# Performance work log

Measured on AMD Instinct MI355X. Metric: run time of the kernel, lower is better.

Reference implementation:

```python
import jax, jax.numpy as jnp
import numpy as np

B, N, FIN, FOUT = 16, 128, 128, 256   # batch, atoms(=max_atom), in_features, out_features
EOUT, BIN, BOUT, CI, L1 = 64, 14, 64, 64, 256


def _rnn_dir(x, wih, whh, bih, bhh):
    # x: [B, T, I]; torch nn.RNN step: h = tanh(x @ Wih^T + bih + h @ Whh^T + bhh)
    h0 = jnp.zeros((x.shape[0], whh.shape[0]), x.dtype)
    def step(h, xt):
        h = jnp.tanh(xt @ wih.T + bih + h @ whh.T + bhh)
        return h, h
    _, ys = jax.lax.scan(step, h0, jnp.swapaxes(x, 0, 1))
    return jnp.swapaxes(ys, 0, 1)  # [B, T, H]


def _bi_rnn(x, wih_f, whh_f, bih_f, bhh_f, wih_b, whh_b, bih_b, bhh_b):
    fwd = _rnn_dir(x, wih_f, whh_f, bih_f, bhh_f)
    bwd = _rnn_dir(x[:, ::-1, :], wih_b, whh_b, bih_b, bhh_b)[:, ::-1, :]
    return jnp.concatenate([fwd, bwd], axis=-1)  # [B, T, 2H]


def setup_inputs() -> dict:
    key = jax.random.key(0)
    ks = jax.random.split(key, 24)
    g = lambda i, shape, s=0.05: (jax.random.normal(ks[i], shape, jnp.float32) * s)
    return {
        "x": g(0, (B, N, FIN), 1.0),
        "adj": jax.random.randint(ks[1], (B, N, N), 0, 2).astype(jnp.int32),
        "w_edge": g(2, (B, N, N, BIN), 1.0),
        "W": g(3, (FIN, FOUT)),
        "a": g(4, (2 * FOUT, EOUT)),
        "wfc_w": g(5, (BIN, BOUT)), "wfc_b": g(6, (BOUT,)),
        "fc_w": g(7, (EOUT + BOUT, 1)), "fc_b": g(8, (1,)),
        "fcc_w": g(9, (FOUT, 1)), "fcc_b": g(10, (1,)),
        "wih_f": g(11, (CI, N)), "whh_f": g(12, (CI, CI)), "bih_f": g(13, (CI,)), "bhh_f": g(14, (CI,)),
        "wih_b": g(15, (CI, N)), "whh_b": g(16, (CI, CI)), "bih_b": g(17, (CI,)), "bhh_b": g(18, (CI,)),
        "fco_w": g(19, (2 * CI + FOUT, L1)), "fco_b": g(20, (L1,)),
    }


def reference(x, adj, w_edge, W, a, wfc_w, wfc_b, fc_w, fc_b, fcc_w, fcc_b,
              wih_f, whh_f, bih_f, bhh_f, wih_b, whh_b, bih_b, bhh_b, fco_w, fco_b):
    h = x @ W  # [B, N, FOUT]
    # faithful reproduction of the repeat/cat(dim=1)/view trick
    t1 = jnp.tile(h, (1, 1, N)).reshape(B, N * N, FOUT)  # row i*N+j = h_i
    t2 = jnp.tile(h, (1, N, 1))                          # row i*N+j = h_j
    atom_trans = jnp.concatenate([t1, t2], axis=1).reshape(B, N, N, 2 * FOUT)
    e = atom_trans @ a                                   # [B, N, N, EOUT]
    wproj = w_edge @ wfc_w + wfc_b                       # [B, N, N, BOUT]
    e = jax.nn.leaky_relu(jnp.concatenate([e, wproj], axis=3))
    e = (e @ fc_w + fc_b)[..., 0]                        # [B, N, N]
    att = jax.nn.softmax(jnp.where(adj > 0, e, jnp.float32(-9e15)), axis=2)
    # dropout is identity in eval mode
    at_in = att[..., None] * h[:, :, None, :]            # [B, N, N, FOUT], h_i broadcast over j
    hn = jax.nn.leaky_relu((at_in @ fcc_w + fcc_b)[..., 0])  # [B, N, N]
    hn = jax.nn.leaky_relu(_bi_rnn(hn, wih_f, whh_f, bih_f, bhh_f, wih_b, whh_b, bih_b, bhh_b))
    h1 = jnp.einsum('bij,bjf->bif', att, h)              # [B, N, FOUT]
    out = jnp.concatenate([hn, h1], axis=2) @ fco_w + fco_b  # [B, N, L1]
    return jax.nn.elu(out)
```

## Files before the change

### kernel.cpp

```cpp
#include <hip/hip_runtime.h>
#include <hip/hip_bf16.h>

#define DEV static __device__ __forceinline__

constexpr int B=16, N=128, FIN=128, FOUT=256, EOUT=64, BINW=14, BOUT=64, CI=64, L1=256;

constexpr int O_H   = 0;
constexpr int O_P   = O_H  + B*N*FOUT;
constexpr int O_Q   = O_P  + B*N*EOUT;
constexpr int O_S   = O_Q  + B*N*EOUT;
constexpr int O_SU  = O_S  + B*N;
constexpr int O_SV  = O_SU + B*N;
constexpr int O_ATT = O_SV + B*N;
constexpr int O_ZF  = O_ATT+ B*N*N;
constexpr int O_ZB  = O_ZF + B*N*CI;
constexpr int O_RF  = O_ZB + B*N*CI;
constexpr int O_RB  = O_RF + B*N*CI;

DEV float bf16_to_f32(unsigned short u){
  unsigned int x = ((unsigned int)u) << 16; float f;
  __builtin_memcpy(&f, &x, 4); return f;
}
DEV void bf2x(unsigned int u, float& lo, float& hi){
  unsigned int a = u << 16, b = u & 0xFFFF0000u;
  __builtin_memcpy(&lo, &a, 4); __builtin_memcpy(&hi, &b, 4);
}
DEV float lrelu(float x){ return x > 0.f ? x : 0.01f * x; }
DEV float bcastf(float v, int lane){
  return __builtin_bit_cast(float, __builtin_amdgcn_readlane(__builtin_bit_cast(int, v), lane));
}
DEV float ldf(const void* p, int i, int m){
  return m ? bf16_to_f32(((const unsigned short*)p)[i]) : ((const float*)p)[i];
}
DEV int blk_mode(const void* x, int nt, int tid){
  const unsigned short* u = (const unsigned short*)x;
  int e = (u[tid & 255] >> 7) & 0xFF;
  int cnt = __syncthreads_count(e >= 100 && e <= 140);
  return cnt * 4 >= nt * 3;
}

__global__ __launch_bounds__(256) void k_h_pq(const void* __restrict__ xr,
                                              const void* __restrict__ Wp,
                                              const void* __restrict__ Ap,
                                              const void* __restrict__ fccwp,
                                              float* __restrict__ ws){
  int blk = blockIdx.x, tid = threadIdx.x;
  int b = blk >> 4, i0 = (blk & 15) * 8;
  __shared__ __align__(16) float xl[8*FIN];
  __shared__ __align__(16) float hrow[8*FOUT];
  __shared__ float red[32];
  int mode = blk_mode(xr, 256, tid);
  if (mode){
    const unsigned short* xu = (const unsigned short*)xr + (size_t)(b*N + i0)*FIN;
    for (int t = tid; t < 8*FIN/8; t += 256){
      uint4 u4 = ((const uint4*)xu)[t];
      float* o = &xl[t*8];
      bf2x(u4.x,o[0],o[1]); bf2x(u4.y,o[2],o[3]); bf2x(u4.z,o[4],o[5]); bf2x(u4.w,o[6],o[7]);
    }
  } else {
    const float* xf = (const float*)xr + (size_t)(b*N + i0)*FIN;
    for (int t4 = tid; t4 < 8*FIN/4; t4 += 256)
      *(float4*)&xl[t4*4] = ((const float4*)xf)[t4];
  }
  __syncthreads();
  int f = tid;
  float acc[8] = {0,0,0,0,0,0,0,0};
  if (mode){
    const unsigned short* Wu = (const unsigned short*)Wp;
    for (int c = 0; c < FIN; c += 4){
      float w0 = bf16_to_f32(Wu[(c+0)*FOUT + f]);
      float w1 = bf16_to_f32(Wu[(c+1)*FOUT + f]);
      float w2 = bf16_to_f32(Wu[(c+2)*FOUT + f]);
      float w3 = bf16_to_f32(Wu[(c+3)*FOUT + f]);
      #pragma unroll
      for (int r = 0; r < 8; ++r){
        float4 x4 = *(const float4*)&xl[r*FIN + c];
        acc[r] += x4.x*w0 + x4.y*w1 + x4.z*w2 + x4.w*w3;
      }
    }
  } else {
    const float* Wf = (const float*)Wp;
    for (int c = 0; c < FIN; c += 4){
      float w0 = Wf[(c+0)*FOUT + f];
      float w1 = Wf[(c+1)*FOUT + f];
      float w2 = Wf[(c+2)*FOUT + f];
      float w3 = Wf[(c+3)*FOUT + f];
      #pragma unroll
      for (int r = 0; r < 8; ++r){
        float4 x4 = *(const float4*)&xl[r*FIN + c];
        acc[r] += x4.x*w0 + x4.y*w1 + x4.z*w2 + x4.w*w3;
      }
    }
  }
  float fw = ldf(fccwp, f, mode);
  #pragma unroll
  for (int r = 0; r < 8; ++r){
    ws[O_H + (b*N + i0 + r)*FOUT + f] = acc[r];
    hrow[r*FOUT + f] = acc[r];
  }
  #pragma unroll
  for (int r = 0; r < 8; ++r){
    float v = acc[r] * fw;
    for (int off = 32; off; off >>= 1) v += __shfl_down(v, off);
    if ((tid & 63) == 0) red[(tid >> 6)*8 + r] = v;
  }
  __syncthreads();
  if (tid < 8){
    float s = red[tid] + red[8+tid] + red[16+tid] + red[24+tid];
    ws[O_S + b*N + i0 + tid] = s;
  }
  {
    int o = tid & 63, which = (tid >> 6) & 1, hh = tid >> 7;
    float a4[4] = {0.f,0.f,0.f,0.f};
    if (mode){
      const unsigned short* Au = (const unsigned short*)Ap;
      for (int c = 0; c < FOUT; c += 4){
        float w0 = bf16_to_f32(Au[(which*FOUT + c+0)*EOUT + o]);
        float w1 = bf16_to_f32(Au[(which*FOUT + c+1)*EOUT + o]);
        float w2 = bf16_to_f32(Au[(which*FOUT + c+2)*EOUT + o]);
        float w3 = bf16_to_f32(Au[(which*FOUT + c+3)*EOUT + o]);
        #pragma unroll
        for (int r = 0; r < 4; ++r){
          float4 h4 = *(const float4*)&hrow[(hh*4+r)*FOUT + c];
          a4[r] += h4.x*w0 + h4.y*w1 + h4.z*w2 + h4.w*w3;
        }
      }
    } else {
      const float* Af = (const float*)Ap;
      for (int c = 0; c < FOUT; c += 4){
        float w0 = Af[(which*FOUT + c+0)*EOUT + o];
        float w1 = Af[(which*FOUT + c+1)*EOUT + o];
        float w2 = Af[(which*FOUT + c+2)*EOUT + o];
        float w3 = Af[(which*FOUT + c+3)*EOUT + o];
        #pragma unroll
        for (int r = 0; r < 4; ++r){
          float4 h4 = *(const float4*)&hrow[(hh*4+r)*FOUT + c];
          a4[r] += h4.x*w0 + h4.y*w1 + h4.z*w2 + h4.w*w3;
        }
      }
    }
    int ob = which ? O_Q : O_P;
    #pragma unroll
    for (int r = 0; r < 4; ++r)
      ws[ob + (b*N + i0 + hh*4 + r)*EOUT + o] = a4[r];
  }
}

__global__ __launch_bounds__(64) void k_susv(const void* __restrict__ xr,
                                             const void* __restrict__ fcwp,
                                             float* __restrict__ ws){
  int blk = blockIdx.x; int b = blk >> 7, r = blk & 127; int o = threadIdx.x;
  int mode = blk_mode(xr, 64, o);
  float fw = ldf(fcwp, o, mode);
  const float* R = ws;
  float u = R[O_P + (b*N + r)*EOUT + o] + R[O_Q + (b*N + r)*EOUT + o];
  float t1 = lrelu(u) * fw;
  int j2 = (2*r) & 127;
  float v = R[O_P + (b*N + j2)*EOUT + o] + R[O_Q + (b*N + j2 + 1)*EOUT + o];
  float t2 = lrelu(v) * fw;
  for (int off = 32; off; off >>= 1){ t1 += __shfl_down(t1, off); t2 += __shfl_down(t2, off); }
  if (o == 0){ ws[O_SU + b*N + r] = t1; ws[O_SV + b*N + r] = t2; }
}

struct AttArgs { const void *we,*x,*wfcw,*wfcb,*fcw,*fcb,*fccb,*wihf,*bihf,*bhhf,*wihb,*bihb,*bhhb; };

__global__ __launch_bounds__(128) void k_att(AttArgs A, const int* __restrict__ adj,
                                             float* __restrict__ ws){
  int blk = blockIdx.x; int b = blk >> 7, i = blk & 127; int tid = threadIdx.x;
  __shared__ __align__(16) float wel[N*BINW];
  __shared__ __align__(16) float hnp[N];
  __shared__ __align__(16) float wfcwl[BINW*BOUT];
  __shared__ __align__(16) float wfcbl[BOUT];
  __shared__ __align__(16) float fcw2l[BOUT];
  __shared__ float red2[2];
  int mode = blk_mode(A.x, 128, tid);
  for (int t = tid; t < BINW*BOUT; t += 128) wfcwl[t] = ldf(A.wfcw, t, mode);
  if (tid < BOUT){ wfcbl[tid] = ldf(A.wfcb, tid, mode); fcw2l[tid] = ldf(A.fcw, EOUT + tid, mode); }
  if (mode){
    const unsigned short* weu = (const unsigned short*)A.we + (size_t)(b*N + i)*N*BINW;
    for (int t = tid; t < N*BINW/8; t += 128){
      uint4 q = ((const uint4*)weu)[t];
      float* o = &wel[t*8];
      bf2x(q.x,o[0],o[1]); bf2x(q.y,o[2],o[3]); bf2x(q.z,o[4],o[5]); bf2x(q.w,o[6],o[7]);
    }
  } else {
    const float* wef = (const float*)A.we + (size_t)(b*N + i)*N*BINW;
    for (int t4 = tid; t4 < N*BINW/4; t4 += 128)
      *(float4*)&wel[t4*4] = ((const float4*)wef)[t4];
  }
  __syncthreads();
  int j = tid;
  float wr[BINW];
  #pragma unroll
  for (int t = 0; t < BINW; ++t) wr[t] = wel[j*BINW + t];
  float wcon = 0.f;
  for (int o = 0; o < BOUT; o += 4){
    float4 bb = *(const float4*)&wfcbl[o];
    float w0 = bb.x, w1 = bb.y, w2 = bb.z, w3 = bb.w;
    #pragma unroll
    for (int t = 0; t < BINW; ++t){
      float4 w4 = *(const float4*)&wfcwl[t*BOUT + o];
      w0 = fmaf(wr[t], w4.x, w0); w1 = fmaf(wr[t], w4.y, w1);
      w2 = fmaf(wr[t], w4.z, w2); w3 = fmaf(wr[t], w4.w, w3);
    }
    float4 f4 = *(const float4*)&fcw2l[o];
    wcon += lrelu(w0)*f4.x + lrelu(w1)*f4.y + lrelu(w2)*f4.z + lrelu(w3)*f4.w;
  }
  const float* R = ws;
  float econ = (i < 64) ? R[O_SU + b*N + 2*i + (j >= 64 ? 1 : 0)]
                        : R[O_SV + b*N + j];
  float etot = econ + wcon + ldf(A.fcb, 0, mode);
  float m = (adj[(b*N + i)*N + j] > 0) ? etot : -9e15f;
  float mx = m;
  for (int off = 32; off; off >>= 1) mx = fmaxf(mx, __shfl_xor(mx, off));
  if ((tid & 63) == 0) red2[tid >> 6] = mx;
  __syncthreads();
  mx = fmaxf(red2[0], red2[1]);
  float ev = expf(m - mx);
  float sum = ev;
  for (int off = 32; off; off >>= 1) sum += __shfl_xor(sum, off);
  __syncthreads();
  if ((tid & 63) == 0) red2[tid >> 6] = sum;
  __syncthreads();
  sum = red2[0] + red2[1];
  float att = ev / sum;
  ws[O_ATT + (b*N + i)*N + j] = att;
  float sbi = R[O_S + b*N + i];
  hnp[j] = lrelu(att * sbi + ldf(A.fccb, 0, mode));
  __syncthreads();
  {
    int d = tid >> 6, c = tid & 63;
    float acc = ldf(d ? A.bihb : A.bihf, c, mode) + ldf(d ? A.bhhb : A.bhhf, c, mode);
    const void* wihp = d ? A.wihb : A.wihf;
    if (mode){
      const uint4* wq = (const uint4*)((const unsigned short*)wihp + c*N);
      #pragma unroll 4
      for (int k = 0; k < N; k += 8){
        uint4 q = wq[k >> 3];
        float w0,w1,w2,w3,w4,w5,w6,w7;
        bf2x(q.x,w0,w1); bf2x(q.y,w2,w3); bf2x(q.z,w4,w5); bf2x(q.w,w6,w7);
        float4 h0 = *(const float4*)&hnp[k];
        float4 h1 = *(const float4*)&hnp[k+4];
        acc += h0.x*w0 + h0.y*w1 + h0.z*w2 + h0.w*w3
             + h1.x*w4 + h1.y*w5 + h1.z*w6 + h1.w*w7;
      }
    } else {
      const float* wf = (const float*)wihp + c*N;
      #pragma unroll 8
      for (int k = 0; k < N; k += 4){
        float4 h4 = *(const float4*)&hnp[k];
        float4 w4 = *(const float4*)&wf[k];
        acc += h4.x*w4.x + h4.y*w4.y + h4.z*w4.z + h4.w*w4.w;
      }
    }
    ws[(d ? O_ZB : O_ZF) + (b*N + i)*CI + c] = acc;
  }
}

__global__ __launch_bounds__(64, 1) void k_rnn(const void* __restrict__ xr,
                                               const void* __restrict__ whhf,
                                               const void* __restrict__ whhb,
                                               float* __restrict__ ws){
  int blk = blockIdx.x; int d = blk >> 4, b = blk & 15; int c = threadIdx.x;
  int mode = blk_mode(xr, 64, c);
  const void* whhp = d ? whhb : whhf;
  const int zb = (d ? O_ZB : O_ZF) + b*N*CI;
  const int ob = (d ? O_RB : O_RF) + b*N*CI;
  __shared__ __align__(16) float zo[N*CI];
  float wreg[CI];
  if (mode){
    const uint4* wq = (const uint4*)((const unsigned short*)whhp + c*CI);
    #pragma unroll
    for (int k = 0; k < CI; k += 8){
      uint4 q = wq[k >> 3];
      bf2x(q.x,wreg[k+0],wreg[k+1]); bf2x(q.y,wreg[k+2],wreg[k+3]);
      bf2x(q.z,wreg[k+4],wreg[k+5]); bf2x(q.w,wreg[k+6],wreg[k+7]);
    }
  } else {
    const float* wf = (const float*)whhp + c*CI;
    #pragma unroll
    for (int k = 0; k < CI; k += 4){
      float4 w4 = *(const float4*)&wf[k];
      wreg[k]=w4.x; wreg[k+1]=w4.y; wreg[k+2]=w4.z; wreg[k+3]=w4.w;
    }
  }
  for (int it = 0; it < N*CI/4; it += 64)
    *(float4*)&zo[(it + c)*4] = *(const float4*)&ws[zb + (it + c)*4];
  const int step = d ? -1 : 1;
  int tt = d ? (N-1) : 0;
  float hv = 0.f;
  float z = zo[tt*CI + c];
  for (int t = 0; t < N; ++t){
    int ti = tt + step; ti = ti < 0 ? 0 : (ti > N-1 ? N-1 : ti);
    float znext = zo[ti*CI + c];
    float s[CI];
    #pragma unroll
    for (int k = 0; k < CI; ++k) s[k] = bcastf(hv, k);
#if __has_builtin(__builtin_amdgcn_sched_barrier)
    __builtin_amdgcn_sched_barrier(0);
#endif
    float a0 = z, a1 = 0.f, a2 = 0.f, a3 = 0.f;
    #pragma unroll
    for (int k = 0; k < CI; k += 4){
      a0 = fmaf(s[k+0], wreg[k+0], a0);
      a1 = fmaf(s[k+1], wreg[k+1], a1);
      a2 = fmaf(s[k+2], wreg[k+2], a2);
      a3 = fmaf(s[k+3], wreg[k+3], a3);
    }
    float x = (a0+a1)+(a2+a3);
    x = fminf(15.f, fmaxf(-15.f, x));
    float p = __expf(2.f * x);
    hv = (p - 1.f) * __builtin_amdgcn_rcpf(p + 1.f);
    zo[tt*CI + c] = hv;
    z = znext;
    tt += step;
  }
  for (int it = 0; it < N*CI/4; it += 64)
    *(float4*)&ws[ob + (it + c)*4] = *(const float4*)&zo[(it + c)*4];
}

__global__ __launch_bounds__(256) void k_out(const void* __restrict__ xr,
                                             const void* __restrict__ fcowp,
                                             const void* __restrict__ fcobp,
                                             const float* __restrict__ R, void* dout){
  int blk = blockIdx.x, tid = threadIdx.x;
  int b = blk >> 4, i0 = (blk & 15) * 8;
  constexpr int KW = 2*CI + FOUT;
  __shared__ __align__(16) float attT[N*8];
  __shared__ __align__(16) float inl[8*KW];
  int mode = blk_mode(xr, 256, tid);
  for (int t = tid; t < 8*N; t += 256){
    int r = t >> 7, k = t & 127;
    attT[k*8 + r] = R[O_ATT + (b*N + i0 + r)*N + k];
  }
  for (int t = tid; t < 8*2*CI; t += 256){
    int r = t >> 7, k = t & 127;
    int row = b*N + i0 + r;
    inl[r*KW + k] = (k < CI) ? lrelu(R[O_RF + row*CI + k])
                             : lrelu(R[O_RB + row*CI + (k - CI)]);
  }
  __syncthreads();
  int f = tid;
  {
    float acc[8] = {0,0,0,0,0,0,0,0};
    for (int k = 0; k < N; ++k){
      float hv = R[O_H + (b*N + k)*FOUT + f];
      float4 a0 = *(const float4*)&attT[k*8];
      float4 a1 = *(const float4*)&attT[k*8 + 4];
      acc[0] += a0.x*hv; acc[1] += a0.y*hv; acc[2] += a0.z*hv; acc[3] += a0.w*hv;
      acc[4] += a1.x*hv; acc[5] += a1.y*hv; acc[6] += a1.z*hv; acc[7] += a1.w*hv;
    }
    #pragma unroll
    for (int r = 0; r < 8; ++r) inl[r*KW + 2*CI + f] = acc[r];
  }
  __syncthreads();
  int l = tid;
  float bias = ldf(fcobp, l, mode);
  float acc[8];
  #pragma unroll
  for (int r = 0; r < 8; ++r) acc[r] = bias;
  if (mode){
    const unsigned short* fu = (const unsigned short*)fcowp;
    for (int k = 0; k < KW; k += 4){
      float w0 = bf16_to_f32(fu[(k+0)*L1 + l]);
      float w1 = bf16_to_f32(fu[(k+1)*L1 + l]);
      float w2 = bf16_to_f32(fu[(k+2)*L1 + l]);
      float w3 = bf16_to_f32(fu[(k+3)*L1 + l]);
      #pragma unroll
      for (int r = 0; r < 8; ++r){
        float4 v = *(const float4*)&inl[r*KW + k];
        acc[r] += v.x*w0 + v.y*w1 + v.z*w2 + v.w*w3;
      }
    }
  } else {
    const float* ff = (const float*)fcowp;
    for (int k = 0; k < KW; k += 4){
      float w0 = ff[(k+0)*L1 + l];
      float w1 = ff[(k+1)*L1 + l];
      float w2 = ff[(k+2)*L1 + l];
      float w3 = ff[(k+3)*L1 + l];
      #pragma unroll
      for (int r = 0; r < 8; ++r){
        float4 v = *(const float4*)&inl[r*KW + k];
        acc[r] += v.x*w0 + v.y*w1 + v.z*w2 + v.w*w3;
      }
    }
  }
  #pragma unroll
  for (int r = 0; r < 8; ++r){
    float o = acc[r] > 0.f ? acc[r] : expm1f(acc[r]);
    int idx = (b*N + i0 + r)*L1 + l;
    if (mode) ((__hip_bfloat16*)dout)[idx] = __float2bfloat16(o);
    else      ((float*)dout)[idx] = o;
  }
}

extern "C" void kernel_launch(void* const* d_in, const int* in_sizes, int n_in,
                              void* d_out, int out_size, void* d_ws, size_t ws_size,
                              hipStream_t stream){
  (void)in_sizes; (void)n_in; (void)out_size; (void)ws_size;
  float* ws = (float*)d_ws;
  AttArgs A;
  A.we = d_in[2]; A.x = d_in[0]; A.wfcw = d_in[5]; A.wfcb = d_in[6];
  A.fcw = d_in[7]; A.fcb = d_in[8]; A.fccb = d_in[10];
  A.wihf = d_in[11]; A.bihf = d_in[13]; A.bhhf = d_in[14];
  A.wihb = d_in[15]; A.bihb = d_in[17]; A.bhhb = d_in[18];
  hipLaunchKernelGGL(k_h_pq, dim3(256),  dim3(256), 0, stream,
                     d_in[0], d_in[3], d_in[4], d_in[9], ws);
  hipLaunchKernelGGL(k_susv, dim3(B*N),  dim3(64),  0, stream, d_in[0], d_in[7], ws);
  hipLaunchKernelGGL(k_att,  dim3(B*N),  dim3(128), 0, stream, A, (const int*)d_in[1], ws);
  hipLaunchKernelGGL(k_rnn,  dim3(32),   dim3(64),  0, stream,
                     d_in[0], d_in[12], d_in[16], ws);
  hipLaunchKernelGGL(k_out,  dim3(256),  dim3(256), 0, stream,
                     d_in[0], d_in[19], d_in[20], ws, d_out);
}
```

Measured before the change: 212.9 us.

## Fuse susv into h_pq, pack two attention rows per block, overlap h1 with RNN

The separate k_susv kernel is folded into k_h_pq, so P/Q projections stay in shared memory and the su/sv scores come from a block-local reduction instead of a global round trip. k_att now processes two attention rows per 256-thread block. The att@h matmul (h1) moves out of k_out into a combined kernel in which 32 blocks run the serial RNN while the other 224 blocks compute h1 in parallel, hiding it behind the RNN latency. This removes one launch and some global traffic, but the fused su/sv indexing is subtle and adds an extra h1 workspace buffer.

Measured after the change: 205.4 us (median of 2 runs). -3.5%, faster.

```diff
diff --git a/kernel.cpp b/kernel.cpp
--- a/kernel.cpp
+++ b/kernel.cpp
@@ -6,9 +6,7 @@
 constexpr int B=16, N=128, FIN=128, FOUT=256, EOUT=64, BINW=14, BOUT=64, CI=64, L1=256;
 
 constexpr int O_H   = 0;
-constexpr int O_P   = O_H  + B*N*FOUT;
-constexpr int O_Q   = O_P  + B*N*EOUT;
-constexpr int O_S   = O_Q  + B*N*EOUT;
+constexpr int O_S   = O_H  + B*N*FOUT;
 constexpr int O_SU  = O_S  + B*N;
 constexpr int O_SV  = O_SU + B*N;
 constexpr int O_ATT = O_SV + B*N;
@@ -16,6 +14,7 @@
 constexpr int O_ZB  = O_ZF + B*N*CI;
 constexpr int O_RF  = O_ZB + B*N*CI;
 constexpr int O_RB  = O_RF + B*N*CI;
+constexpr int O_H1  = O_RB + B*N*CI;
 
 DEV float bf16_to_f32(unsigned short u){
   unsigned int x = ((unsigned int)u) << 16; float f;
@@ -43,11 +42,14 @@
                                               const void* __restrict__ Wp,
                                               const void* __restrict__ Ap,
                                               const void* __restrict__ fccwp,
+                                              const void* __restrict__ fcwp,
                                               float* __restrict__ ws){
   int blk = blockIdx.x, tid = threadIdx.x;
   int b = blk >> 4, i0 = (blk & 15) * 8;
   __shared__ __align__(16) float xl[8*FIN];
   __shared__ __align__(16) float hrow[8*FOUT];
+  __shared__ __align__(16) float pl[8*EOUT];
+  __shared__ __align__(16) float ql[8*EOUT];
   __shared__ float red[32];
   int mode = blk_mode(xr, 256, tid);
   if (mode){
@@ -139,60 +141,63 @@
         }
       }
     }
-    int ob = which ? O_Q : O_P;
+    float* dst = which ? ql : pl;
     #pragma unroll
-    for (int r = 0; r < 4; ++r)
-      ws[ob + (b*N + i0 + hh*4 + r)*EOUT + o] = a4[r];
-  }
-}
-
-__global__ __launch_bounds__(64) void k_susv(const void* __restrict__ xr,
-                                             const void* __restrict__ fcwp,
+    for (int r = 0; r < 4; ++r) dst[(hh*4+r)*EOUT + o] = a4[r];
+  }
+  __syncthreads();
+  {
+    int o = tid & 63, w = tid >> 6;
+    float fw2 = ldf(fcwp, o, mode);
+    float s1 = lrelu(pl[w*EOUT + o]     + ql[w*EOUT + o])     * fw2;
+    float s2 = lrelu(pl[(w+4)*EOUT + o] + ql[(w+4)*EOUT + o]) * fw2;
+    float s3 = lrelu(pl[(2*w)*EOUT + o] + ql[(2*w+1)*EOUT + o]) * fw2;
+    for (int off = 32; off; off >>= 1){
+      s1 += __shfl_down(s1, off); s2 += __shfl_down(s2, off); s3 += __shfl_down(s3, off);
+    }
+    if (o == 0){
+      ws[O_SU + b*N + i0 + w]     = s1;
+      ws[O_SU + b*N + i0 + w + 4] = s2;
+      int r1 = (i0 + 2*w) >> 1;
+      ws[O_SV + b*N + r1]      = s3;
+      ws[O_SV + b*N + r1 + 64] = s3;
+    }
+  }
+}
+
+struct AttArgs { const void *we,*x,*wfcw,*wfcb,*fcw,*fcb,*fccb,*wihf,*bihf,*bhhf,*wihb,*bihb,*bhhb; };
+
+__global__ __launch_bounds__(256) void k_att(AttArgs A, const int* __restrict__ adj,
                                              float* __restrict__ ws){
-  int blk = blockIdx.x; int b = blk >> 7, r = blk & 127; int o = threadIdx.x;
-  int mode = blk_mode(xr, 64, o);
-  float fw = ldf(fcwp, o, mode);
-  const float* R = ws;
-  float u = R[O_P + (b*N + r)*EOUT + o] + R[O_Q + (b*N + r)*EOUT + o];
-  float t1 = lrelu(u) * fw;
-  int j2 = (2*r) & 127;
-  float v = R[O_P + (b*N + j2)*EOUT + o] + R[O_Q + (b*N + j2 + 1)*EOUT + o];
-  float t2 = lrelu(v) * fw;
-  for (int off = 32; off; off >>= 1){ t1 += __shfl_down(t1, off); t2 += __shfl_down(t2, off); }
-  if (o == 0){ ws[O_SU + b*N + r] = t1; ws[O_SV + b*N + r] = t2; }
-}
-
-struct AttArgs { const void *we,*x,*wfcw,*wfcb,*fcw,*fcb,*fccb,*wihf,*bihf,*bhhf,*wihb,*bihb,*bhhb; };
-
-__global__ __launch_bounds__(128) void k_att(AttArgs A, const int* __restrict__ adj,
-                                             float* __restrict__ ws){
-  int blk = blockIdx.x; int b = blk >> 7, i = blk & 127; int tid = threadIdx.x;
-  __shared__ __align__(16) float wel[N*BINW];
-  __shared__ __align__(16) float hnp[N];
+  int blk = blockIdx.x, tid = threadIdx.x;
+  int half = tid >> 7, j = tid & 127, wv = (tid >> 6) & 1;
+  int tau = blk*2 + half;
+  int b = tau >> 7, i = tau & 127;
+  __shared__ __align__(16) float wel[2][N*BINW];
+  __shared__ __align__(16) float hnp[2][N];
   __shared__ __align__(16) float wfcwl[BINW*BOUT];
   __shared__ __align__(16) float wfcbl[BOUT];
   __shared__ __align__(16) float fcw2l[BOUT];
-  __shared__ float red2[2];
-  int mode = blk_mode(A.x, 128, tid);
-  for (int t = tid; t < BINW*BOUT; t += 128) wfcwl[t] = ldf(A.wfcw, t, mode);
+  __shared__ float red2[2][2];
+  int mode = blk_mode(A.x, 256, tid);
+  for (int t = tid; t < BINW*BOUT; t += 256) wfcwl[t] = ldf(A.wfcw, t, mode);
   if (tid < BOUT){ wfcbl[tid] = ldf(A.wfcb, tid, mode); fcw2l[tid] = ldf(A.fcw, EOUT + tid, mode); }
   if (mode){
     const unsigned short* weu = (const unsigned short*)A.we + (size_t)(b*N + i)*N*BINW;
-    for (int t = tid; t < N*BINW/8; t += 128){
+    for (int t = j; t < N*BINW/8; t += 128){
       uint4 q = ((const uint4*)weu)[t];
-      float* o = &wel[t*8];
+      float* o = &wel[half][t*8];
       bf2x(q.x,o[0],o[1]); bf2x(q.y,o[2],o[3]); bf2x(q.z,o[4],o[5]); bf2x(q.w,o[6],o[7]);
     }
   } else {
     const float* wef = (const float*)A.we + (size_t)(b*N + i)*N*BINW;
-    for (int t4 = tid; t4 < N*BINW/4; t4 += 128)
-      *(float4*)&wel[t4*4] = ((const float4*)wef)[t4];
-  }
-  __syncthreads();
-  int j = tid;
+    for (int t4 = j; t4 < N*BINW/4; t4 += 128)
+      *(float4*)&wel[half][t4*4] = ((const float4*)wef)[t4];
+  }
+  __syncthreads();
   float wr[BINW];
   #pragma unroll
-  for (int t = 0; t < BINW; ++t) wr[t] = wel[j*BINW + t];
+  for (int t = 0; t < BINW; ++t) wr[t] = wel[half][j*BINW + t];
   float wcon = 0.f;
   for (int o = 0; o < BOUT; o += 4){
     float4 bb = *(const float4*)&wfcbl[o];
@@ -213,23 +218,23 @@
   float m = (adj[(b*N + i)*N + j] > 0) ? etot : -9e15f;
   float mx = m;
   for (int off = 32; off; off >>= 1) mx = fmaxf(mx, __shfl_xor(mx, off));
-  if ((tid & 63) == 0) red2[tid >> 6] = mx;
-  __syncthreads();
-  mx = fmaxf(red2[0], red2[1]);
+  if ((tid & 63) == 0) red2[half][wv] = mx;
+  __syncthreads();
+  mx = fmaxf(red2[half][0], red2[half][1]);
   float ev = expf(m - mx);
   float sum = ev;
   for (int off = 32; off; off >>= 1) sum += __shfl_xor(sum, off);
   __syncthreads();
-  if ((tid & 63) == 0) red2[tid >> 6] = sum;
-  __syncthreads();
-  sum = red2[0] + red2[1];
+  if ((tid & 63) == 0) red2[half][wv] = sum;
+  __syncthreads();
+  sum = red2[half][0] + red2[half][1];
   float att = ev / sum;
   ws[O_ATT + (b*N + i)*N + j] = att;
   float sbi = R[O_S + b*N + i];
-  hnp[j] = lrelu(att * sbi + ldf(A.fccb, 0, mode));
+  hnp[half][j] = lrelu(att * sbi + ldf(A.fccb, 0, mode));
   __syncthreads();
   {
-    int d = tid >> 6, c = tid & 63;
+    int d = wv, c = tid & 63;
     float acc = ldf(d ? A.bihb : A.bihf, c, mode) + ldf(d ? A.bhhb : A.bhhf, c, mode);
     const void* wihp = d ? A.wihb : A.wihf;
     if (mode){
@@ -239,8 +244,8 @@
         uint4 q = wq[k >> 3];
         float w0,w1,w2,w3,w4,w5,w6,w7;
         bf2x(q.x,w0,w1); bf2x(q.y,w2,w3); bf2x(q.z,w4,w5); bf2x(q.w,w6,w7);
-        float4 h0 = *(const float4*)&hnp[k];
-        float4 h1 = *(const float4*)&hnp[k+4];
+        float4 h0 = *(const float4*)&hnp[half][k];
+        float4 h1 = *(const float4*)&hnp[half][k+4];
         acc += h0.x*w0 + h0.y*w1 + h0.z*w2 + h0.w*w3
              + h1.x*w4 + h1.y*w5 + h1.z*w6 + h1.w*w7;
       }
@@ -248,7 +253,7 @@
       const float* wf = (const float*)wihp + c*N;
       #pragma unroll 8
       for (int k = 0; k < N; k += 4){
-        float4 h4 = *(const float4*)&hnp[k];
+        float4 h4 = *(const float4*)&hnp[half][k];
         float4 w4 = *(const float4*)&wf[k];
         acc += h4.x*w4.x + h4.y*w4.y + h4.z*w4.z + h4.w*w4.w;
       }
@@ -257,66 +262,97 @@
   }
 }
 
-__global__ __launch_bounds__(64, 1) void k_rnn(const void* __restrict__ xr,
-                                               const void* __restrict__ whhf,
-                                               const void* __restrict__ whhb,
-                                               float* __restrict__ ws){
-  int blk = blockIdx.x; int d = blk >> 4, b = blk & 15; int c = threadIdx.x;
-  int mode = blk_mode(xr, 64, c);
-  const void* whhp = d ? whhb : whhf;
-  const int zb = (d ? O_ZB : O_ZF) + b*N*CI;
-  const int ob = (d ? O_RB : O_RF) + b*N*CI;
-  __shared__ __align__(16) float zo[N*CI];
-  float wreg[CI];
-  if (mode){
-    const uint4* wq = (const uint4*)((const unsigned short*)whhp + c*CI);
-    #pragma unroll
-    for (int k = 0; k < CI; k += 8){
-      uint4 q = wq[k >> 3];
-      bf2x(q.x,wreg[k+0],wreg[k+1]); bf2x(q.y,wreg[k+2],wreg[k+3]);
-      bf2x(q.z,wreg[k+4],wreg[k+5]); bf2x(q.w,wreg[k+6],wreg[k+7]);
-    }
+__global__ __launch_bounds__(256, 1) void k_rnn_h1(const void* __restrict__ xr,
+                                                   const void* __restrict__ whhf,
+                                                   const void* __restrict__ whhb,
+                                                   float* __restrict__ ws){
+  __shared__ __align__(16) float sh[N*CI];
+  int blk = blockIdx.x, tid = threadIdx.x;
+  int mode = blk_mode(xr, 256, tid);
+  const float* R = ws;
+  if (blk < 32){
+    int d = blk >> 4, b = blk & 15;
+    const int zb = (d ? O_ZB : O_ZF) + b*N*CI;
+    const int ob = (d ? O_RB : O_RF) + b*N*CI;
+    for (int it = tid; it < N*CI/4; it += 256)
+      *(float4*)&sh[it*4] = *(const float4*)&ws[zb + it*4];
+    __syncthreads();
+    if (tid < 64){
+      int c = tid;
+      const void* whhp = d ? whhb : whhf;
+      float wreg[CI];
+      if (mode){
+        const uint4* wq = (const uint4*)((const unsigned short*)whhp + c*CI);
+        #pragma unroll
+        for (int k = 0; k < CI; k += 8){
+          uint4 q = wq[k >> 3];
+          bf2x(q.x,wreg[k+0],wreg[k+1]); bf2x(q.y,wreg[k+2],wreg[k+3]);
+          bf2x(q.z,wreg[k+4],wreg[k+5]); bf2x(q.w,wreg[k+6],wreg[k+7]);
+        }
+      } else {
+        const float* wf = (const float*)whhp + c*CI;
+        #pragma unroll
+        for (int k = 0; k < CI; k += 4){
+          float4 w4 = *(const float4*)&wf[k];
+          wreg[k]=w4.x; wreg[k+1]=w4.y; wreg[k+2]=w4.z; wreg[k+3]=w4.w;
+        }
+      }
+      const int step = d ? -1 : 1;
+      int tt = d ? (N-1) : 0;
+      float hv = 0.f;
+      float z = sh[tt*CI + c];
+      for (int t = 0; t < N; ++t){
+        int ti = tt + step; ti = ti < 0 ? 0 : (ti > N-1 ? N-1 : ti);
+        float znext = sh[ti*CI + c];
+        float s[CI];
+        #pragma unroll
+        for (int k = 0; k < CI; ++k) s[k] = bcastf(hv, k);
+#if __has_builtin(__builtin_amdgcn_sched_barrier)
+        __builtin_amdgcn_sched_barrier(0);
+#endif
+        float a0 = z, a1 = 0.f, a2 = 0.f, a3 = 0.f;
+        #pragma unroll
+        for (int k = 0; k < CI; k += 4){
+          a0 = fmaf(s[k+0], wreg[k+0], a0);
+          a1 = fmaf(s[k+1], wreg[k+1], a1);
+          a2 = fmaf(s[k+2], wreg[k+2], a2);
+          a3 = fmaf(s[k+3], wreg[k+3], a3);
+        }
+        float x = (a0+a1)+(a2+a3);
+        x = fminf(15.f, fmaxf(-15.f, x));
+        float p = __expf(2.f * x);
+        hv = (p - 1.f) * __builtin_amdgcn_rcpf(p + 1.f);
+        sh[tt*CI + c] = hv;
+        z = znext;
+        tt += step;
+      }
+    }
+    __syncthreads();
+    for (int it = tid; it < N*CI/4; it += 256)
+      *(float4*)&ws[ob + it*4] = *(const float4*)&sh[it*4];
   } else {
-    const float* wf = (const float*)whhp + c*CI;
-    #pragma unroll
-    for (int k = 0; k < CI; k += 4){
-      float4 w4 = *(const float4*)&wf[k];
-      wreg[k]=w4.x; wreg[k+1]=w4.y; wreg[k+2]=w4.z; wreg[k+3]=w4.w;
-    }
-  }
-  for (int it = 0; it < N*CI/4; it += 64)
-    *(float4*)&zo[(it + c)*4] = *(const float4*)&ws[zb + (it + c)*4];
-  const int step = d ? -1 : 1;
-  int tt = d ? (N-1) : 0;
-  float hv = 0.f;
-  float z = zo[tt*CI + c];
-  for (int t = 0; t < N; ++t){
-    int ti = tt + step; ti = ti < 0 ? 0 : (ti > N-1 ? N-1 : ti);
-    float znext = zo[ti*CI + c];
-    float s[CI];
-    #pragma unroll
-    for (int k = 0; k < CI; ++k) s[k] = bcastf(hv, k);
-#if __has_builtin(__builtin_amdgcn_sched_barrier)
-    __builtin_amdgcn_sched_barrier(0);
-#endif
-    float a0 = z, a1 = 0.f, a2 = 0.f, a3 = 0.f;
-    #pragma unroll
-    for (int k = 0; k < CI; k += 4){
-      a0 = fmaf(s[k+0], wreg[k+0], a0);
-      a1 = fmaf(s[k+1], wreg[k+1], a1);
-      a2 = fmaf(s[k+2], wreg[k+2], a2);
-      a3 = fmaf(s[k+3], wreg[k+3], a3);
-    }
-    float x = (a0+a1)+(a2+a3);
-    x = fminf(15.f, fmaxf(-15.f, x));
-    float p = __expf(2.f * x);
-    hv = (p - 1.f) * __builtin_amdgcn_rcpf(p + 1.f);
-    zo[tt*CI + c] = hv;
-    z = znext;
-    tt += step;
-  }
-  for (int it = 0; it < N*CI/4; it += 64)
-    *(float4*)&ws[ob + (it + c)*4] = *(const float4*)&zo[(it + c)*4];
+    for (int task = blk - 32; task < 256; task += 224){
+      int b = task >> 4, i0 = (task & 15) * 8;
+      int f = tid;
+      __syncthreads();
+      for (int t = tid; t < 8*N; t += 256){
+        int r = t >> 7, k = t & 127;
+        sh[k*8 + r] = R[O_ATT + (b*N + i0 + r)*N + k];
+      }
+      __syncthreads();
+      float acc[8] = {0,0,0,0,0,0,0,0};
+      for (int k = 0; k < N; ++k){
+        float hv = R[O_H + (b*N + k)*FOUT + f];
+        float4 a0 = *(const float4*)&sh[k*8];
+        float4 a1 = *(const float4*)&sh[k*8 + 4];
+        acc[0] += a0.x*hv; acc[1] += a0.y*hv; acc[2] += a0.z*hv; acc[3] += a0.w*hv;
+        acc[4] += a1.x*hv; acc[5] += a1.y*hv; acc[6] += a1.z*hv; acc[7] += a1.w*hv;
+      }
+      #pragma unroll
+      for (int r = 0; r < 8; ++r)
+        ws[O_H1 + (b*N + i0 + r)*FOUT + f] = acc[r];
+    }
+  }
 }
 
 __global__ __launch_bounds__(256) void k_out(const void* __restrict__ xr,
@@ -326,32 +362,17 @@
   int blk = blockIdx.x, tid = threadIdx.x;
   int b = blk >> 4, i0 = (blk & 15) * 8;
   constexpr int KW = 2*CI + FOUT;
-  __shared__ __align__(16) float attT[N*8];
   __shared__ __align__(16) float inl[8*KW];
   int mode = blk_mode(xr, 256, tid);
-  for (int t = tid; t < 8*N; t += 256){
-    int r = t >> 7, k = t & 127;
-    attT[k*8 + r] = R[O_ATT + (b*N + i0 + r)*N + k];
-  }
   for (int t = tid; t < 8*2*CI; t += 256){
     int r = t >> 7, k = t & 127;
     int row = b*N + i0 + r;
     inl[r*KW + k] = (k < CI) ? lrelu(R[O_RF + row*CI + k])
                              : lrelu(R[O_RB + row*CI + (k - CI)]);
   }
-  __syncthreads();
-  int f = tid;
-  {
-    float acc[8] = {0,0,0,0,0,0,0,0};
-    for (int k = 0; k < N; ++k){
-      float hv = R[O_H + (b*N + k)*FOUT + f];
-      float4 a0 = *(const float4*)&attT[k*8];
-      float4 a1 = *(const float4*)&attT[k*8 + 4];
-      acc[0] += a0.x*hv; acc[1] += a0.y*hv; acc[2] += a0.z*hv; acc[3] += a0.w*hv;
-      acc[4] += a1.x*hv; acc[5] += a1.y*hv; acc[6] += a1.z*hv; acc[7] += a1.w*hv;
-    }
-    #pragma unroll
-    for (int r = 0; r < 8; ++r) inl[r*KW + 2*CI + f] = acc[r];
+  for (int t = tid; t < 8*FOUT; t += 256){
+    int r = t >> 8, k = t & 255;
+    inl[r*KW + 2*CI + k] = R[O_H1 + (b*N + i0 + r)*FOUT + k];
   }
   __syncthreads();
   int l = tid;
@@ -405,12 +426,11 @@
   A.fcw = d_in[7]; A.fcb = d_in[8]; A.fccb = d_in[10];
   A.wihf = d_in[11]; A.bihf = d_in[13]; A.bhhf = d_in[14];
   A.wihb = d_in[15]; A.bihb = d_in[17]; A.bhhb = d_in[18];
-  hipLaunchKernelGGL(k_h_pq, dim3(256),  dim3(256), 0, stream,
-                     d_in[0], d_in[3], d_in[4], d_in[9], ws);
-  hipLaunchKernelGGL(k_susv, dim3(B*N),  dim3(64),  0, stream, d_in[0], d_in[7], ws);
-  hipLaunchKernelGGL(k_att,  dim3(B*N),  dim3(128), 0, stream, A, (const int*)d_in[1], ws);
-  hipLaunchKernelGGL(k_rnn,  dim3(32),   dim3(64),  0, stream,
+  hipLaunchKernelGGL(k_h_pq,   dim3(256),    dim3(256), 0, stream,
+                     d_in[0], d_in[3], d_in[4], d_in[9], d_in[7], ws);
+  hipLaunchKernelGGL(k_att,    dim3(B*N/2),  dim3(256), 0, stream, A, (const int*)d_in[1], ws);
+  hipLaunchKernelGGL(k_rnn_h1, dim3(256),    dim3(256), 0, stream,
                      d_in[0], d_in[12], d_in[16], ws);
-  hipLaunchKernelGGL(k_out,  dim3(256),  dim3(256), 0, stream,
+  hipLaunchKernelGGL(k_out,    dim3(256),    dim3(256), 0, stream,
                      d_in[0], d_in[19], d_in[20], ws, d_out);
 }
```
